# Optimization experiments

Measured on AMD Instinct MI355X. Metric: run time of the kernel, lower is better.

The kernel has to match this reference:

```python
import jax, jax.numpy as jnp
import numpy as np

N_NODES = 100000
N_EDGES = 600000
IN_CH = 128
HID = 128


def setup_inputs() -> dict:
    key = jax.random.key(0)
    ks = jax.random.split(key, 8)
    x = jax.random.normal(ks[0], (N_NODES, IN_CH), dtype=jnp.float32)
    edge_index = jax.random.randint(ks[1], (2, N_EDGES), 0, N_NODES, dtype=jnp.int64)
    # Linear weights stored as (in, out); scaled like torch default init
    W1 = jax.random.normal(ks[2], (2 * IN_CH, HID), dtype=jnp.float32) / np.sqrt(2 * IN_CH)
    b1 = jnp.zeros((HID,), dtype=jnp.float32)
    W2 = jax.random.normal(ks[3], (HID, HID), dtype=jnp.float32) / np.sqrt(HID)
    b2 = jnp.zeros((HID,), dtype=jnp.float32)
    W3 = jax.random.normal(ks[4], (HID, 1), dtype=jnp.float32) / np.sqrt(HID)
    b3 = jnp.zeros((1,), dtype=jnp.float32)
    return {"x": x, "edge_index": edge_index, "W1": W1, "b1": b1,
            "W2": W2, "b2": b2, "W3": W3, "b3": b3}


def reference(x, edge_index, W1, b1, W2, b2, W3, b3):
    src = edge_index[0]
    tgt = edge_index[1]
    # gather + concat: [n_edges, 2*in_channels]
    h = jnp.concatenate([x[src, :], x[tgt, :]], axis=1)
    h = jax.nn.elu(h @ W1 + b1)
    h = jax.nn.elu(h @ W2 + b2)
    h = h @ W3 + b3  # [n_edges, 1]
    return jnp.squeeze(h)  # squeeze=True path -> [n_edges]
```

## Files before the change

### kernel.cpp

```cpp
#include <hip/hip_runtime.h>

#define N_NODES 100000
#define N_EDGES 600000
#define NT1 782
#define NT2 4688
#define LDH 136
#define G1H 512

typedef _Float16 f16x8 __attribute__((ext_vector_type(8)));
typedef __attribute__((ext_vector_type(4))) float f32x4;

__device__ __forceinline__ float elu_f(float v) {
    return v > 0.0f ? v : (__expf(v) - 1.0f);
}

extern "C" __global__ void k_detect(const unsigned* __restrict__ ei, int* __restrict__ flag) {
    int t = threadIdx.x;
    unsigned v = ei[2 * t + 1];
    unsigned long long b = __ballot(v == 0u);
    if (t == 0) *flag = (b == ~0ull) ? 1 : 0;
}

extern "C" __global__ __launch_bounds__(256, 4)
void k1_node_linear(const float* __restrict__ x, const float* __restrict__ W1,
                    _Float16* __restrict__ P) {
    __shared__ __align__(16) _Float16 sX[128 * LDH];

    const int t = threadIdx.x;
    const int w = t >> 6, lane = t & 63;
    const int ln = lane & 15, kg = lane >> 4;
    const int kcf = t & 15;
    const int lef = t >> 4;
    const int half = (blockIdx.x >= G1H) ? 1 : 0;
    const int t0 = blockIdx.x - half * G1H;

    f16x8 bf[2][4];
#pragma unroll
    for (int c = 0; c < 2; ++c) {
        const int n = w * 32 + c * 16 + ln;
#pragma unroll
        for (int ks = 0; ks < 4; ++ks) {
            f16x8 v;
#pragma unroll
            for (int j = 0; j < 8; ++j) {
                int k = half * 128 + ks * 32 + kg * 8 + j;
                v[j] = (_Float16)W1[k * 128 + n];
            }
            bf[c][ks] = v;
        }
    }

    for (int tile = t0; tile < NT1; tile += G1H) {
        const int n0 = tile * 128;
        __syncthreads();
#pragma unroll 2
        for (int r = 0; r < 8; ++r) {
            int le = r * 16 + lef;
            int n = n0 + le;
            float4 a0 = make_float4(0.f, 0.f, 0.f, 0.f), a1 = a0;
            if (n < N_NODES) {
                const float* p = x + (size_t)n * 128 + kcf * 8;
                a0 = *(const float4*)p; a1 = *(const float4*)(p + 4);
            }
            float f[8] = {a0.x, a0.y, a0.z, a0.w, a1.x, a1.y, a1.z, a1.w};
            f16x8 vh;
#pragma unroll
            for (int j = 0; j < 8; ++j) vh[j] = (_Float16)f[j];
            *(f16x8*)(&sX[le * LDH + kcf * 8]) = vh;
        }
        __syncthreads();

        f32x4 acc[8][2];
#pragma unroll
        for (int rt = 0; rt < 8; ++rt)
#pragma unroll
            for (int c = 0; c < 2; ++c) acc[rt][c] = (f32x4){0.f, 0.f, 0.f, 0.f};

#pragma unroll
        for (int ks = 0; ks < 4; ++ks) {
#pragma unroll
            for (int rt = 0; rt < 8; ++rt) {
                f16x8 a = *(const f16x8*)(&sX[(rt * 16 + ln) * LDH + ks * 32 + kg * 8]);
#pragma unroll
                for (int c = 0; c < 2; ++c)
                    acc[rt][c] = __builtin_amdgcn_mfma_f32_16x16x32_f16(a, bf[c][ks], acc[rt][c], 0, 0, 0);
            }
        }

        __syncthreads();
#pragma unroll
        for (int rt = 0; rt < 8; ++rt)
#pragma unroll
            for (int c = 0; c < 2; ++c) {
                int col = w * 32 + c * 16 + ln;
#pragma unroll
                for (int reg = 0; reg < 4; ++reg) {
                    int row = rt * 16 + kg * 4 + reg;
                    sX[row * LDH + col] = (_Float16)acc[rt][c][reg];
                }
            }
        __syncthreads();
        {
            int row_l = t >> 1, seg = t & 1;
            int n = n0 + row_l;
            if (n < N_NODES) {
                _Float16* dst = P + (size_t)n * 256 + half * 128 + seg * 64;
                const _Float16* srcp = &sX[row_l * LDH + seg * 64];
#pragma unroll
                for (int i = 0; i < 8; ++i)
                    *(f16x8*)(dst + i * 8) = *(const f16x8*)(srcp + i * 8);
            }
        }
    }
}

extern "C" __global__ __launch_bounds__(256, 4)
void k2_edge_mlp(const _Float16* __restrict__ P, const void* __restrict__ eiv,
                 const float* __restrict__ b1, const float* __restrict__ W2,
                 const float* __restrict__ b2, const float* __restrict__ W3,
                 const float* __restrict__ b3, const int* __restrict__ flag,
                 float* __restrict__ out) {
    __shared__ __align__(16) _Float16 sH[128 * LDH];
    __shared__ float sPart[4 * 128];
    __shared__ int sSrc[128], sTgt[128];

    const int t = threadIdx.x;
    const int w = t >> 6, lane = t & 63;
    const int ln = lane & 15, kg = lane >> 4;
    const int kcf = t & 15;
    const int lef = t >> 4;
    const int mode64 = *flag;
    const float b3v = b3[0];

    float b1v[8];
#pragma unroll
    for (int j = 0; j < 8; ++j) b1v[j] = b1[kcf * 8 + j];
    float w3v[2], b2v[2];
#pragma unroll
    for (int c = 0; c < 2; ++c) {
        int col = w * 32 + c * 16 + ln;
        w3v[c] = W3[col]; b2v[c] = b2[col];
    }

    f16x8 bf[2][4];
#pragma unroll
    for (int c = 0; c < 2; ++c) {
        const int n = w * 32 + c * 16 + ln;
#pragma unroll
        for (int ks = 0; ks < 4; ++ks) {
            f16x8 v;
#pragma unroll
            for (int j = 0; j < 8; ++j) {
                int k = ks * 32 + kg * 8 + j;
                v[j] = (_Float16)W2[k * 128 + n];
            }
            bf[c][ks] = v;
        }
    }

    int tile = blockIdx.x;
    if (t < 128 && tile < NT2) {
        int e = tile * 128 + t;
        int s = 0, g = 0;
        if (e < N_EDGES) {
            if (mode64) {
                s = (int)((const long long*)eiv)[e];
                g = (int)((const long long*)eiv)[N_EDGES + e];
            } else {
                s = ((const int*)eiv)[e];
                g = ((const int*)eiv)[N_EDGES + e];
            }
        }
        sSrc[t] = s; sTgt[t] = g;
    }
    __syncthreads();

    for (; tile < NT2; tile += gridDim.x) {
        const int e0 = tile * 128;

#pragma unroll 2
        for (int r = 0; r < 8; ++r) {
            int le = r * 16 + lef;
            int s = sSrc[le], g = sTgt[le];
            f16x8 a8 = *(const f16x8*)(P + (size_t)s * 256 + kcf * 8);
            f16x8 c8 = *(const f16x8*)(P + (size_t)g * 256 + 128 + kcf * 8);
            f16x8 vh;
#pragma unroll
            for (int j = 0; j < 8; ++j) {
                float hv = elu_f((float)a8[j] + (float)c8[j] + b1v[j]);
                vh[j] = (_Float16)hv;
            }
            *(f16x8*)(&sH[le * LDH + kcf * 8]) = vh;
        }
        __syncthreads();

        f32x4 acc[8][2];
#pragma unroll
        for (int rt = 0; rt < 8; ++rt)
#pragma unroll
            for (int c = 0; c < 2; ++c) acc[rt][c] = (f32x4){0.f, 0.f, 0.f, 0.f};

#pragma unroll
        for (int ks = 0; ks < 4; ++ks) {
#pragma unroll
            for (int rt = 0; rt < 8; ++rt) {
                f16x8 a = *(const f16x8*)(&sH[(rt * 16 + ln) * LDH + ks * 32 + kg * 8]);
#pragma unroll
                for (int c = 0; c < 2; ++c)
                    acc[rt][c] = __builtin_amdgcn_mfma_f32_16x16x32_f16(a, bf[c][ks], acc[rt][c], 0, 0, 0);
            }
        }

#pragma unroll
        for (int rt = 0; rt < 8; ++rt) {
            float p[4] = {0.f, 0.f, 0.f, 0.f};
#pragma unroll
            for (int c = 0; c < 2; ++c) {
#pragma unroll
                for (int reg = 0; reg < 4; ++reg)
                    p[reg] += elu_f(acc[rt][c][reg] + b2v[c]) * w3v[c];
            }
#pragma unroll
            for (int m = 1; m < 16; m <<= 1)
#pragma unroll
                for (int reg = 0; reg < 4; ++reg) p[reg] += __shfl_xor(p[reg], m, 64);
            if (ln == 0) {
#pragma unroll
                for (int reg = 0; reg < 4; ++reg)
                    sPart[w * 128 + rt * 16 + kg * 4 + reg] = p[reg];
            }
        }
        __syncthreads();

        if (t < 128) {
            int e = e0 + t;
            if (e < N_EDGES)
                out[e] = sPart[t] + sPart[128 + t] + sPart[256 + t] + sPart[384 + t] + b3v;
            int nt = tile + gridDim.x;
            if (nt < NT2) {
                int en = nt * 128 + t;
                int s = 0, g = 0;
                if (en < N_EDGES) {
                    if (mode64) {
                        s = (int)((const long long*)eiv)[en];
                        g = (int)((const long long*)eiv)[N_EDGES + en];
                    } else {
                        s = ((const int*)eiv)[en];
                        g = ((const int*)eiv)[N_EDGES + en];
                    }
                }
                sSrc[t] = s; sTgt[t] = g;
            }
        }
        __syncthreads();
    }
}

extern "C" void kernel_launch(void* const* d_in, const int* in_sizes, int n_in,
                              void* d_out, int out_size, void* d_ws, size_t ws_size,
                              hipStream_t stream) {
    const float* x  = (const float*)d_in[0];
    const void*  ei = d_in[1];
    const float* W1 = (const float*)d_in[2];
    const float* b1 = (const float*)d_in[3];
    const float* W2 = (const float*)d_in[4];
    const float* b2 = (const float*)d_in[5];
    const float* W3 = (const float*)d_in[6];
    const float* b3 = (const float*)d_in[7];
    float* out = (float*)d_out;

    int* flag = (int*)d_ws;
    _Float16* P = (_Float16*)((char*)d_ws + 256);

    k_detect<<<1, 64, 0, stream>>>((const unsigned*)ei, flag);
    k1_node_linear<<<1024, 256, 0, stream>>>(x, W1, P);
    k2_edge_mlp<<<1024, 256, 0, stream>>>(P, ei, b1, W2, b2, W3, b3, flag, out);
}
```

Measured before the change: 222.0 us.

## Prefetch next tile's gathered node rows into registers during MFMA stage

The edge kernel now double-buffers edge indices in shared memory and issues the gathers of P rows for the next tile into registers before running the current tile's MFMA and epilogue, so gather latency overlaps compute. The MFMA stage is split into two halves to limit accumulator register pressure, and launch bounds drop to 3 waves per SIMD. The separate index-width detect kernel is removed and done per block inside the edge kernel, saving one launch. The costs are a larger register footprint from the 16 prefetch vectors and lower occupancy.

```diff
diff --git a/kernel.cpp b/kernel.cpp
--- a/kernel.cpp
+++ b/kernel.cpp
@@ -12,13 +12,6 @@
 
 __device__ __forceinline__ float elu_f(float v) {
     return v > 0.0f ? v : (__expf(v) - 1.0f);
-}
-
-extern "C" __global__ void k_detect(const unsigned* __restrict__ ei, int* __restrict__ flag) {
-    int t = threadIdx.x;
-    unsigned v = ei[2 * t + 1];
-    unsigned long long b = __ballot(v == 0u);
-    if (t == 0) *flag = (b == ~0ull) ? 1 : 0;
 }
 
 extern "C" __global__ __launch_bounds__(256, 4)
@@ -114,23 +107,28 @@
     }
 }
 
-extern "C" __global__ __launch_bounds__(256, 4)
+extern "C" __global__ __launch_bounds__(256, 3)
 void k2_edge_mlp(const _Float16* __restrict__ P, const void* __restrict__ eiv,
                  const float* __restrict__ b1, const float* __restrict__ W2,
                  const float* __restrict__ b2, const float* __restrict__ W3,
-                 const float* __restrict__ b3, const int* __restrict__ flag,
-                 float* __restrict__ out) {
+                 const float* __restrict__ b3, float* __restrict__ out) {
     __shared__ __align__(16) _Float16 sH[128 * LDH];
     __shared__ float sPart[4 * 128];
-    __shared__ int sSrc[128], sTgt[128];
+    __shared__ int sSrc[2][128], sTgt[2][128];
+    __shared__ int sFlag;
 
     const int t = threadIdx.x;
     const int w = t >> 6, lane = t & 63;
     const int ln = lane & 15, kg = lane >> 4;
     const int kcf = t & 15;
     const int lef = t >> 4;
-    const int mode64 = *flag;
     const float b3v = b3[0];
+
+    if (t < 64) {
+        unsigned v = ((const unsigned*)eiv)[2 * t + 1];
+        unsigned long long bm = __ballot(v == 0u);
+        if (t == 0) sFlag = (bm == ~0ull) ? 1 : 0;
+    }
 
     float b1v[8];
 #pragma unroll
@@ -157,8 +155,11 @@
             bf[c][ks] = v;
         }
     }
+    __syncthreads();
+    const int mode64 = sFlag;
 
     int tile = blockIdx.x;
+    int par = 0;
     if (t < 128 && tile < NT2) {
         int e = tile * 128 + t;
         int s = 0, g = 0;
@@ -171,9 +172,20 @@
                 g = ((const int*)eiv)[N_EDGES + e];
             }
         }
-        sSrc[t] = s; sTgt[t] = g;
+        sSrc[0][t] = s; sTgt[0][t] = g;
     }
     __syncthreads();
+
+    f16x8 Ga[8], Gb[8];
+    if (tile < NT2) {
+#pragma unroll
+        for (int r = 0; r < 8; ++r) {
+            int le = r * 16 + lef;
+            int s = sSrc[0][le], g = sTgt[0][le];
+            Ga[r] = *(const f16x8*)(P + (size_t)s * 256 + kcf * 8);
+            Gb[r] = *(const f16x8*)(P + (size_t)g * 256 + 128 + kcf * 8);
+        }
+    }
 
     for (; tile < NT2; tile += gridDim.x) {
         const int e0 = tile * 128;
@@ -181,53 +193,80 @@
 #pragma unroll 2
         for (int r = 0; r < 8; ++r) {
             int le = r * 16 + lef;
-            int s = sSrc[le], g = sTgt[le];
-            f16x8 a8 = *(const f16x8*)(P + (size_t)s * 256 + kcf * 8);
-            f16x8 c8 = *(const f16x8*)(P + (size_t)g * 256 + 128 + kcf * 8);
             f16x8 vh;
 #pragma unroll
             for (int j = 0; j < 8; ++j) {
-                float hv = elu_f((float)a8[j] + (float)c8[j] + b1v[j]);
+                float hv = elu_f((float)Ga[r][j] + (float)Gb[r][j] + b1v[j]);
                 vh[j] = (_Float16)hv;
             }
             *(f16x8*)(&sH[le * LDH + kcf * 8]) = vh;
         }
-        __syncthreads();
-
-        f32x4 acc[8][2];
-#pragma unroll
-        for (int rt = 0; rt < 8; ++rt)
-#pragma unroll
-            for (int c = 0; c < 2; ++c) acc[rt][c] = (f32x4){0.f, 0.f, 0.f, 0.f};
-
-#pragma unroll
-        for (int ks = 0; ks < 4; ++ks) {
-#pragma unroll
-            for (int rt = 0; rt < 8; ++rt) {
-                f16x8 a = *(const f16x8*)(&sH[(rt * 16 + ln) * LDH + ks * 32 + kg * 8]);
-#pragma unroll
-                for (int c = 0; c < 2; ++c)
-                    acc[rt][c] = __builtin_amdgcn_mfma_f32_16x16x32_f16(a, bf[c][ks], acc[rt][c], 0, 0, 0);
-            }
-        }
-
-#pragma unroll
-        for (int rt = 0; rt < 8; ++rt) {
-            float p[4] = {0.f, 0.f, 0.f, 0.f};
-#pragma unroll
-            for (int c = 0; c < 2; ++c) {
-#pragma unroll
-                for (int reg = 0; reg < 4; ++reg)
-                    p[reg] += elu_f(acc[rt][c][reg] + b2v[c]) * w3v[c];
-            }
-#pragma unroll
-            for (int m = 1; m < 16; m <<= 1)
-#pragma unroll
-                for (int reg = 0; reg < 4; ++reg) p[reg] += __shfl_xor(p[reg], m, 64);
-            if (ln == 0) {
-#pragma unroll
-                for (int reg = 0; reg < 4; ++reg)
-                    sPart[w * 128 + rt * 16 + kg * 4 + reg] = p[reg];
+
+        const int nt = tile + gridDim.x;
+        if (t < 128 && nt < NT2) {
+            int e = nt * 128 + t;
+            int s = 0, g = 0;
+            if (e < N_EDGES) {
+                if (mode64) {
+                    s = (int)((const long long*)eiv)[e];
+                    g = (int)((const long long*)eiv)[N_EDGES + e];
+                } else {
+                    s = ((const int*)eiv)[e];
+                    g = ((const int*)eiv)[N_EDGES + e];
+                }
+            }
+            sSrc[par ^ 1][t] = s; sTgt[par ^ 1][t] = g;
+        }
+        __syncthreads();
+
+        if (nt < NT2) {
+#pragma unroll
+            for (int r = 0; r < 8; ++r) {
+                int le = r * 16 + lef;
+                int s = sSrc[par ^ 1][le], g = sTgt[par ^ 1][le];
+                Ga[r] = *(const f16x8*)(P + (size_t)s * 256 + kcf * 8);
+                Gb[r] = *(const f16x8*)(P + (size_t)g * 256 + 128 + kcf * 8);
+            }
+        }
+
+#pragma unroll
+        for (int rh = 0; rh < 2; ++rh) {
+            f32x4 acc[4][2];
+#pragma unroll
+            for (int rt = 0; rt < 4; ++rt)
+#pragma unroll
+                for (int c = 0; c < 2; ++c) acc[rt][c] = (f32x4){0.f, 0.f, 0.f, 0.f};
+
+#pragma unroll
+            for (int ks = 0; ks < 4; ++ks) {
+#pragma unroll
+                for (int rt = 0; rt < 4; ++rt) {
+                    int row = (rh * 4 + rt) * 16 + ln;
+                    f16x8 a = *(const f16x8*)(&sH[row * LDH + ks * 32 + kg * 8]);
+#pragma unroll
+                    for (int c = 0; c < 2; ++c)
+                        acc[rt][c] = __builtin_amdgcn_mfma_f32_16x16x32_f16(a, bf[c][ks], acc[rt][c], 0, 0, 0);
+                }
+            }
+
+#pragma unroll
+            for (int rt = 0; rt < 4; ++rt) {
+                float p[4] = {0.f, 0.f, 0.f, 0.f};
+#pragma unroll
+                for (int c = 0; c < 2; ++c) {
+#pragma unroll
+                    for (int reg = 0; reg < 4; ++reg)
+                        p[reg] += elu_f(acc[rt][c][reg] + b2v[c]) * w3v[c];
+                }
+#pragma unroll
+                for (int m = 1; m < 16; m <<= 1)
+#pragma unroll
+                    for (int reg = 0; reg < 4; ++reg) p[reg] += __shfl_xor(p[reg], m, 64);
+                if (ln == 0) {
+#pragma unroll
+                    for (int reg = 0; reg < 4; ++reg)
+                        sPart[w * 128 + (rh * 4 + rt) * 16 + kg * 4 + reg] = p[reg];
+                }
             }
         }
         __syncthreads();
@@ -236,23 +275,9 @@
             int e = e0 + t;
             if (e < N_EDGES)
                 out[e] = sPart[t] + sPart[128 + t] + sPart[256 + t] + sPart[384 + t] + b3v;
-            int nt = tile + gridDim.x;
-            if (nt < NT2) {
-                int en = nt * 128 + t;
-                int s = 0, g = 0;
-                if (en < N_EDGES) {
-                    if (mode64) {
-                        s = (int)((const long long*)eiv)[en];
-                        g = (int)((const long long*)eiv)[N_EDGES + en];
-                    } else {
-                        s = ((const int*)eiv)[en];
-                        g = ((const int*)eiv)[N_EDGES + en];
-                    }
-                }
-                sSrc[t] = s; sTgt[t] = g;
-            }
-        }
-        __syncthreads();
+        }
+        __syncthreads();
+        par ^= 1;
     }
 }
 
@@ -269,10 +294,8 @@
     const float* b3 = (const float*)d_in[7];
     float* out = (float*)d_out;
 
-    int* flag = (int*)d_ws;
     _Float16* P = (_Float16*)((char*)d_ws + 256);
 
-    k_detect<<<1, 64, 0, stream>>>((const unsigned*)ei, flag);
     k1_node_linear<<<1024, 256, 0, stream>>>(x, W1, P);
-    k2_edge_mlp<<<1024, 256, 0, stream>>>(P, ei, b1, W2, b2, W3, b3, flag, out);
+    k2_edge_mlp<<<1024, 256, 0, stream>>>(P, ei, b1, W2, b2, W3, b3, out);
 }
```

Measured after the change: 495.3 us. 2.23x slower.

## Restructure edge MLP so each wave owns edges and reads W2 from shared memory

Applied to the files above, without the earlier changes.

Each wave now gathers its own 32 edges directly into MFMA A-fragments in registers, adding the two projections with the bias and applying ELU in fp16. This removes the shared-memory staging of the hidden layer and the per-tile block barriers. W2 is transposed into LDS once per block and read as B-fragments. Each wave covers all 128 output columns, so the cross-wave partial-sum reduction goes away. The separate index-width detect kernel is folded into the edge kernel, the launch bound drops to 3 blocks per CU, and the grid grows to 1172. In exchange, the first-layer bias add and its sum are computed in fp16 and register pressure rises.

```diff
diff --git a/kernel.cpp b/kernel.cpp
--- a/kernel.cpp
+++ b/kernel.cpp
@@ -12,13 +12,6 @@
 
 __device__ __forceinline__ float elu_f(float v) {
     return v > 0.0f ? v : (__expf(v) - 1.0f);
-}
-
-extern "C" __global__ void k_detect(const unsigned* __restrict__ ei, int* __restrict__ flag) {
-    int t = threadIdx.x;
-    unsigned v = ei[2 * t + 1];
-    unsigned long long b = __ballot(v == 0u);
-    if (t == 0) *flag = (b == ~0ull) ? 1 : 0;
 }
 
 extern "C" __global__ __launch_bounds__(256, 4)
@@ -114,111 +107,114 @@
     }
 }
 
-extern "C" __global__ __launch_bounds__(256, 4)
+extern "C" __global__ __launch_bounds__(256, 3)
 void k2_edge_mlp(const _Float16* __restrict__ P, const void* __restrict__ eiv,
                  const float* __restrict__ b1, const float* __restrict__ W2,
                  const float* __restrict__ b2, const float* __restrict__ W3,
-                 const float* __restrict__ b3, const int* __restrict__ flag,
-                 float* __restrict__ out) {
-    __shared__ __align__(16) _Float16 sH[128 * LDH];
-    __shared__ float sPart[4 * 128];
-    __shared__ int sSrc[128], sTgt[128];
+                 const float* __restrict__ b3, float* __restrict__ out) {
+    __shared__ __align__(16) _Float16 sW2T[128 * LDH];
+    __shared__ int sFlag;
 
     const int t = threadIdx.x;
     const int w = t >> 6, lane = t & 63;
     const int ln = lane & 15, kg = lane >> 4;
-    const int kcf = t & 15;
-    const int lef = t >> 4;
-    const int mode64 = *flag;
     const float b3v = b3[0];
 
-    float b1v[8];
-#pragma unroll
-    for (int j = 0; j < 8; ++j) b1v[j] = b1[kcf * 8 + j];
-    float w3v[2], b2v[2];
-#pragma unroll
-    for (int c = 0; c < 2; ++c) {
-        int col = w * 32 + c * 16 + ln;
-        w3v[c] = W3[col]; b2v[c] = b2[col];
-    }
-
-    f16x8 bf[2][4];
-#pragma unroll
-    for (int c = 0; c < 2; ++c) {
-        const int n = w * 32 + c * 16 + ln;
+    if (t < 64) {
+        unsigned v = ((const unsigned*)eiv)[2 * t + 1];
+        unsigned long long bm = __ballot(v == 0u);
+        if (t == 0) sFlag = (bm == ~0ull) ? 1 : 0;
+    }
+
+#pragma unroll 4
+    for (int r = 0; r < 64; ++r) {
+        int idx = r * 256 + t;
+        int k = idx >> 7, n = idx & 127;
+        sW2T[n * LDH + k] = (_Float16)W2[k * 128 + n];
+    }
+
+    f16x8 b1f[4];
+#pragma unroll
+    for (int ks = 0; ks < 4; ++ks)
+#pragma unroll
+        for (int j = 0; j < 8; ++j) b1f[ks][j] = (_Float16)b1[ks * 32 + kg * 8 + j];
+    float w3v[8], b2v[8];
+#pragma unroll
+    for (int cg = 0; cg < 8; ++cg) {
+        int col = cg * 16 + ln;
+        w3v[cg] = W3[col]; b2v[cg] = b2[col];
+    }
+    __syncthreads();
+    const int mode64 = sFlag;
+
+    for (int tile = blockIdx.x; tile < NT2; tile += gridDim.x) {
+        const int ebase = tile * 128 + w * 32;
+
+        int se[2], ge[2];
+#pragma unroll
+        for (int rg = 0; rg < 2; ++rg) {
+            int e = ebase + rg * 16 + ln;
+            int s = 0, g = 0;
+            if (e < N_EDGES) {
+                if (mode64) {
+                    s = (int)((const long long*)eiv)[e];
+                    g = (int)((const long long*)eiv)[N_EDGES + e];
+                } else {
+                    s = ((const int*)eiv)[e];
+                    g = ((const int*)eiv)[N_EDGES + e];
+                }
+            }
+            se[rg] = s; ge[rg] = g;
+        }
+
+        f16x8 A[2][4];
+#pragma unroll
+        for (int rg = 0; rg < 2; ++rg) {
+            const _Float16* pa = P + (size_t)se[rg] * 256 + kg * 8;
+            const _Float16* pb = P + (size_t)ge[rg] * 256 + 128 + kg * 8;
+            f16x8 Ga[4], Gb[4];
+#pragma unroll
+            for (int ks = 0; ks < 4; ++ks) {
+                Ga[ks] = *(const f16x8*)(pa + ks * 32);
+                Gb[ks] = *(const f16x8*)(pb + ks * 32);
+            }
+#pragma unroll
+            for (int ks = 0; ks < 4; ++ks) {
+                f16x8 s = Ga[ks] + Gb[ks] + b1f[ks];
+                f16x8 vh;
+#pragma unroll
+                for (int j = 0; j < 8; ++j)
+                    vh[j] = (_Float16)elu_f((float)s[j]);
+                A[rg][ks] = vh;
+            }
+        }
+
+        f32x4 acc0[8], acc1[8];
+#pragma unroll
+        for (int cg = 0; cg < 8; ++cg) {
+            acc0[cg] = (f32x4){0.f, 0.f, 0.f, 0.f};
+            acc1[cg] = (f32x4){0.f, 0.f, 0.f, 0.f};
+        }
 #pragma unroll
         for (int ks = 0; ks < 4; ++ks) {
-            f16x8 v;
-#pragma unroll
-            for (int j = 0; j < 8; ++j) {
-                int k = ks * 32 + kg * 8 + j;
-                v[j] = (_Float16)W2[k * 128 + n];
-            }
-            bf[c][ks] = v;
-        }
-    }
-
-    int tile = blockIdx.x;
-    if (t < 128 && tile < NT2) {
-        int e = tile * 128 + t;
-        int s = 0, g = 0;
-        if (e < N_EDGES) {
-            if (mode64) {
-                s = (int)((const long long*)eiv)[e];
-                g = (int)((const long long*)eiv)[N_EDGES + e];
-            } else {
-                s = ((const int*)eiv)[e];
-                g = ((const int*)eiv)[N_EDGES + e];
-            }
-        }
-        sSrc[t] = s; sTgt[t] = g;
-    }
-    __syncthreads();
-
-    for (; tile < NT2; tile += gridDim.x) {
-        const int e0 = tile * 128;
-
-#pragma unroll 2
-        for (int r = 0; r < 8; ++r) {
-            int le = r * 16 + lef;
-            int s = sSrc[le], g = sTgt[le];
-            f16x8 a8 = *(const f16x8*)(P + (size_t)s * 256 + kcf * 8);
-            f16x8 c8 = *(const f16x8*)(P + (size_t)g * 256 + 128 + kcf * 8);
-            f16x8 vh;
-#pragma unroll
-            for (int j = 0; j < 8; ++j) {
-                float hv = elu_f((float)a8[j] + (float)c8[j] + b1v[j]);
-                vh[j] = (_Float16)hv;
-            }
-            *(f16x8*)(&sH[le * LDH + kcf * 8]) = vh;
-        }
-        __syncthreads();
-
-        f32x4 acc[8][2];
-#pragma unroll
-        for (int rt = 0; rt < 8; ++rt)
-#pragma unroll
-            for (int c = 0; c < 2; ++c) acc[rt][c] = (f32x4){0.f, 0.f, 0.f, 0.f};
-
-#pragma unroll
-        for (int ks = 0; ks < 4; ++ks) {
-#pragma unroll
-            for (int rt = 0; rt < 8; ++rt) {
-                f16x8 a = *(const f16x8*)(&sH[(rt * 16 + ln) * LDH + ks * 32 + kg * 8]);
-#pragma unroll
-                for (int c = 0; c < 2; ++c)
-                    acc[rt][c] = __builtin_amdgcn_mfma_f32_16x16x32_f16(a, bf[c][ks], acc[rt][c], 0, 0, 0);
-            }
-        }
-
-#pragma unroll
-        for (int rt = 0; rt < 8; ++rt) {
+#pragma unroll
+            for (int cg = 0; cg < 8; ++cg) {
+                f16x8 bfr = *(const f16x8*)(&sW2T[(cg * 16 + ln) * LDH + ks * 32 + kg * 8]);
+                acc0[cg] = __builtin_amdgcn_mfma_f32_16x16x32_f16(A[0][ks], bfr, acc0[cg], 0, 0, 0);
+                acc1[cg] = __builtin_amdgcn_mfma_f32_16x16x32_f16(A[1][ks], bfr, acc1[cg], 0, 0, 0);
+            }
+        }
+
+#pragma unroll
+        for (int rg = 0; rg < 2; ++rg) {
             float p[4] = {0.f, 0.f, 0.f, 0.f};
 #pragma unroll
-            for (int c = 0; c < 2; ++c) {
-#pragma unroll
-                for (int reg = 0; reg < 4; ++reg)
-                    p[reg] += elu_f(acc[rt][c][reg] + b2v[c]) * w3v[c];
+            for (int cg = 0; cg < 8; ++cg) {
+#pragma unroll
+                for (int reg = 0; reg < 4; ++reg) {
+                    float h = (rg == 0 ? acc0[cg][reg] : acc1[cg][reg]) + b2v[cg];
+                    p[reg] += elu_f(h) * w3v[cg];
+                }
             }
 #pragma unroll
             for (int m = 1; m < 16; m <<= 1)
@@ -226,33 +222,12 @@
                 for (int reg = 0; reg < 4; ++reg) p[reg] += __shfl_xor(p[reg], m, 64);
             if (ln == 0) {
 #pragma unroll
-                for (int reg = 0; reg < 4; ++reg)
-                    sPart[w * 128 + rt * 16 + kg * 4 + reg] = p[reg];
-            }
-        }
-        __syncthreads();
-
-        if (t < 128) {
-            int e = e0 + t;
-            if (e < N_EDGES)
-                out[e] = sPart[t] + sPart[128 + t] + sPart[256 + t] + sPart[384 + t] + b3v;
-            int nt = tile + gridDim.x;
-            if (nt < NT2) {
-                int en = nt * 128 + t;
-                int s = 0, g = 0;
-                if (en < N_EDGES) {
-                    if (mode64) {
-                        s = (int)((const long long*)eiv)[en];
-                        g = (int)((const long long*)eiv)[N_EDGES + en];
-                    } else {
-                        s = ((const int*)eiv)[en];
-                        g = ((const int*)eiv)[N_EDGES + en];
-                    }
-                }
-                sSrc[t] = s; sTgt[t] = g;
-            }
-        }
-        __syncthreads();
+                for (int reg = 0; reg < 4; ++reg) {
+                    int e = ebase + rg * 16 + kg * 4 + reg;
+                    if (e < N_EDGES) out[e] = p[reg] + b3v;
+                }
+            }
+        }
     }
 }
 
@@ -269,10 +244,8 @@
     const float* b3 = (const float*)d_in[7];
     float* out = (float*)d_out;
 
-    int* flag = (int*)d_ws;
     _Float16* P = (_Float16*)((char*)d_ws + 256);
 
-    k_detect<<<1, 64, 0, stream>>>((const unsigned*)ei, flag);
     k1_node_linear<<<1024, 256, 0, stream>>>(x, W1, P);
-    k2_edge_mlp<<<1024, 256, 0, stream>>>(P, ei, b1, W2, b2, W3, b3, flag, out);
-}
+    k2_edge_mlp<<<1172, 256, 0, stream>>>(P, ei, b1, W2, b2, W3, b3, out);
+}
```

Result: slower. 328.3 us (+47.9%).
